# Kernel optimization log

Measured on AMD Instinct MI355X. Metric: run time of the kernel, lower is better.

## Reference

```python
import jax, jax.numpy as jnp
import numpy as np

B, C, L, N = 2, 8, 128, 48  # volume side L, kept size N per axis (fact=4 -> N >= L/4)


def setup_inputs() -> dict:
    key = jax.random.key(0)
    ks = jax.random.split(key, 7)
    x = jax.random.normal(ks[0], (B, C, L, L, L), dtype=jnp.float32)
    EN3 = jax.random.normal(ks[1], (L, N), dtype=jnp.float32)
    EN2 = jax.random.normal(ks[2], (L, N), dtype=jnp.float32)
    EN1 = jax.random.normal(ks[3], (L, N), dtype=jnp.float32)
    DE3 = jax.random.normal(ks[4], (N, L), dtype=jnp.float32)
    DE2 = jax.random.normal(ks[5], (N, L), dtype=jnp.float32)
    DE1 = jax.random.normal(ks[6], (N, L), dtype=jnp.float32)
    return {"x": x, "EN3": EN3, "EN2": EN2, "EN1": EN1,
            "DE3": DE3, "DE2": DE2, "DE1": DE1}


def reference(x, EN3, EN2, EN1, DE3, DE2, DE1):
    # ---- encode: contract D (axis -3) with EN3, H (axis -2) with EN2, W (axis -1) with EN1
    e = jnp.einsum('bcdhw,dp->bcphw', x, EN3)
    e = jnp.einsum('bcphw,hq->bcpqw', e, EN2)
    enc = jnp.einsum('bcpqw,wr->bcpqr', e, EN1)  # (B,C,N,N,N)
    # ---- decode: three application orders of DE1/DE2/DE3, averaged (as in source)
    # order W,H,D
    y = jnp.einsum('bcpqr,rw->bcpqw', enc, DE1)
    y = jnp.einsum('bcpqw,qh->bcphw', y, DE2)
    y1 = jnp.einsum('bcphw,pd->bcdhw', y, DE3)
    # order H,D,W
    y = jnp.einsum('bcpqr,qh->bcphr', enc, DE2)
    y = jnp.einsum('bcphr,pd->bcdhr', y, DE3)
    y2 = jnp.einsum('bcdhr,rw->bcdhw', y, DE1)
    # order D,W,H
    y = jnp.einsum('bcpqr,pd->bcdqr', enc, DE3)
    y = jnp.einsum('bcdqr,rw->bcdqw', y, DE1)
    y3 = jnp.einsum('bcdqw,qh->bcdhw', y, DE2)
    return (y1 + y2 + y3) / 3.0
```

## Files before the change

### kernel.cpp

```cpp
#include <hip/hip_runtime.h>


#define LDIM 128
#define NDIM 48
#define HW   (LDIM * LDIM)
#define L3V  (LDIM * HW)
#define QR   2304

typedef __bf16 bf16x8 __attribute__((ext_vector_type(8)));
typedef float  f32x4  __attribute__((ext_vector_type(4)));
typedef unsigned short u16;

#define S128 136
#define S64  72

#define W_EN3T 0
#define W_EN2T 6144
#define W_EN1T 12288
#define W_DE3T 18432
#define W_DE2T 26624
#define W_DE1T 34816
#define W_M    43008
#define W_TOT  59392

__device__ __forceinline__ u16 f2bf(float f) {
    unsigned int u = __builtin_bit_cast(unsigned int, f);
    return (u16)((u + 0x7fffu + ((u >> 16) & 1u)) >> 16);
}
__device__ __forceinline__ bf16x8 frag(const u16* p) {
    return *reinterpret_cast<const bf16x8*>(p);
}
__device__ __forceinline__ f32x4 mfma16(bf16x8 a, bf16x8 b, f32x4 c) {
    return __builtin_amdgcn_mfma_f32_16x16x32_bf16(a, b, c, 0, 0, 0);
}

__global__ __launch_bounds__(256) void kPrep(const float* __restrict__ EN3,
                                             const float* __restrict__ EN2,
                                             const float* __restrict__ EN1,
                                             const float* __restrict__ DE3,
                                             const float* __restrict__ DE2,
                                             const float* __restrict__ DE1,
                                             u16* __restrict__ W) {
    int i = blockIdx.x * 256 + threadIdx.x;
    if (i < 6144)       { int p = i >> 7, d = i & 127;                 W[i] = f2bf(EN3[d * 48 + p]); }
    else if (i < 12288) { int j = i - 6144;  int q = j >> 7, h = j & 127; W[i] = f2bf(EN2[h * 48 + q]); }
    else if (i < 18432) { int j = i - 12288; int r = j >> 7, w = j & 127; W[i] = f2bf(EN1[w * 48 + r]); }
    else if (i < 26624) { int j = i - 18432; int d = j >> 6, p = j & 63;  W[i] = f2bf(p < 48 ? DE3[p * 128 + d] : 0.f); }
    else if (i < 34816) { int j = i - 26624; int h = j >> 6, q = j & 63;  W[i] = f2bf(q < 48 ? DE2[q * 128 + h] : 0.f); }
    else if (i < 43008) { int j = i - 34816; int w = j >> 6, r = j & 63;  W[i] = f2bf(r < 48 ? DE1[r * 128 + w] : 0.f); }
    else if (i < 59392) {
        int j = i - 43008; int dp = j >> 7, d = j & 127;
        float s = 0.f;
        for (int p = 0; p < 48; ++p) s += EN3[d * 48 + p] * DE3[p * 128 + dp];
        W[i] = f2bf(s);
    }
}

__global__ __launch_bounds__(256) void kEnc(const float* __restrict__ x,
                                            const u16* __restrict__ W,
                                            u16* __restrict__ t) {
    __shared__ u16 lS[128 * S128];
    __shared__ u16 lT[48 * S128];
    const int bc = blockIdx.y, d = blockIdx.x;
    const int tid = threadIdx.x, lane = tid & 63, wv = tid >> 6, quad = lane >> 4;
    const int row = lane & 15, kof = quad * 8;

    {
        const float* xp = x + (size_t)bc * L3V + (size_t)d * HW;
        for (int i = 0; i < 16; ++i) {
            int f = i * 1024 + tid * 4;
            float4 v = *reinterpret_cast<const float4*>(xp + f);
            int h = f >> 7, w = f & 127;
            uint2 pk;
            pk.x = (unsigned)f2bf(v.x) | ((unsigned)f2bf(v.y) << 16);
            pk.y = (unsigned)f2bf(v.z) | ((unsigned)f2bf(v.w) << 16);
            *reinterpret_cast<uint2*>(lS + h * S128 + w) = pk;
        }
    }
    __syncthreads();
    {
        const int h0 = wv * 32;
        f32x4 acc[2][3] = {};
        for (int kk = 0; kk < 4; ++kk) {
            bf16x8 b[3];
            for (int n = 0; n < 3; ++n)
                b[n] = frag(W + W_EN1T + (n * 16 + row) * 128 + kk * 32 + kof);
            for (int m = 0; m < 2; ++m) {
                bf16x8 a = frag(lS + (h0 + m * 16 + row) * S128 + kk * 32 + kof);
                for (int n = 0; n < 3; ++n) acc[m][n] = mfma16(a, b[n], acc[m][n]);
            }
        }
        for (int m = 0; m < 2; ++m)
            for (int n = 0; n < 3; ++n) {
                int r = n * 16 + row, h = h0 + m * 16 + quad * 4;
                uint2 pk;
                pk.x = (unsigned)f2bf(acc[m][n][0]) | ((unsigned)f2bf(acc[m][n][1]) << 16);
                pk.y = (unsigned)f2bf(acc[m][n][2]) | ((unsigned)f2bf(acc[m][n][3]) << 16);
                *reinterpret_cast<uint2*>(lT + r * S128 + h) = pk;
            }
    }
    __syncthreads();
    if (wv < 3) {
        const int q0 = wv * 16;
        f32x4 acc[3] = {};
        for (int kk = 0; kk < 4; ++kk) {
            bf16x8 a = frag(W + W_EN2T + (q0 + row) * 128 + kk * 32 + kof);
            for (int n = 0; n < 3; ++n) {
                bf16x8 b = frag(lT + (n * 16 + row) * S128 + kk * 32 + kof);
                acc[n] = mfma16(a, b, acc[n]);
            }
        }
        u16* tp = t + (size_t)(bc * 128 + d) * QR;
        for (int n = 0; n < 3; ++n)
            for (int j = 0; j < 4; ++j)
                tp[(q0 + quad * 4 + j) * 48 + n * 16 + row] = f2bf(acc[n][j]);
    }
}

__global__ __launch_bounds__(256) void kM(const u16* __restrict__ t,
                                          const u16* __restrict__ W,
                                          u16* __restrict__ u) {
    __shared__ u16 lB[64 * S128];
    const int bc = blockIdx.y, qr0 = blockIdx.x * 64;
    const int tid = threadIdx.x, lane = tid & 63, wv = tid >> 6, quad = lane >> 4;
    const int row = lane & 15, kof = quad * 8;

    {
        const u16* tp = t + (size_t)bc * (128 * QR) + qr0 + (tid & 7) * 8;
        const int d0 = tid >> 3;
        for (int g = 0; g < 4; ++g) {
            int dd = d0 + g * 32;
            u16 v[8];
            *reinterpret_cast<float4*>(v) = *reinterpret_cast<const float4*>(tp + (size_t)dd * QR);
            for (int j = 0; j < 8; ++j) lB[((tid & 7) * 8 + j) * S128 + dd] = v[j];
        }
    }
    __syncthreads();
    const int m0 = wv * 32;
    f32x4 acc[2][4] = {};
    for (int kk = 0; kk < 4; ++kk) {
        bf16x8 a[2], b[4];
        for (int n = 0; n < 4; ++n)
            b[n] = frag(lB + (n * 16 + row) * S128 + kk * 32 + kof);
        for (int m = 0; m < 2; ++m)
            a[m] = frag(W + W_M + (m0 + m * 16 + row) * 128 + kk * 32 + kof);
        for (int m = 0; m < 2; ++m)
            for (int n = 0; n < 4; ++n) acc[m][n] = mfma16(a[m], b[n], acc[m][n]);
    }
    u16* up = u + (size_t)bc * (128 * QR) + qr0;
    for (int m = 0; m < 2; ++m)
        for (int n = 0; n < 4; ++n)
            for (int j = 0; j < 4; ++j) {
                int dp = m0 + m * 16 + quad * 4 + j;
                up[(size_t)dp * QR + n * 16 + row] = f2bf(acc[m][n][j]);
            }
}

__global__ __launch_bounds__(256) void kDec(const u16* __restrict__ u,
                                            const u16* __restrict__ W,
                                            float* __restrict__ out) {
    __shared__ u16 lU[48 * S64];
    __shared__ u16 lV[128 * S64];
    const int bc = blockIdx.y, dp = blockIdx.x;
    const int tid = threadIdx.x, lane = tid & 63, wv = tid >> 6, quad = lane >> 4;
    const int row = lane & 15, kof = quad * 8;

    for (int i = tid; i < 48 * 16; i += 256)  lU[(i >> 4) * S64 + 48 + (i & 15)] = 0;
    for (int i = tid; i < 128 * 16; i += 256) lV[(i >> 4) * S64 + 48 + (i & 15)] = 0;
    {
        const u16* sp = u + (size_t)(bc * 128 + dp) * QR;
        for (int i = tid; i < 288; i += 256) {
            u16 v[8];
            *reinterpret_cast<float4*>(v) = *reinterpret_cast<const float4*>(sp + i * 8);
            int q = i / 6, rb = (i % 6) * 8;
            for (int j = 0; j < 8; ++j) lU[(rb + j) * S64 + q] = v[j];
        }
    }
    __syncthreads();
    {
        const int h0 = wv * 32;
        f32x4 acc[2][3] = {};
        for (int kk = 0; kk < 2; ++kk) {
            bf16x8 b[3];
            for (int n = 0; n < 3; ++n)
                b[n] = frag(lU + (n * 16 + row) * S64 + kk * 32 + kof);
            for (int m = 0; m < 2; ++m) {
                bf16x8 a = frag(W + W_DE2T + (h0 + m * 16 + row) * 64 + kk * 32 + kof);
                for (int n = 0; n < 3; ++n) acc[m][n] = mfma16(a, b[n], acc[m][n]);
            }
        }
        for (int m = 0; m < 2; ++m)
            for (int n = 0; n < 3; ++n)
                for (int j = 0; j < 4; ++j)
                    lV[(h0 + m * 16 + quad * 4 + j) * S64 + n * 16 + row] = f2bf(acc[m][n][j]);
    }
    __syncthreads();
    {
        const int h0 = wv * 32;
        f32x4 acc[2][8] = {};
        for (int kk = 0; kk < 2; ++kk) {
            bf16x8 a[2], b[8];
            for (int n = 0; n < 8; ++n)
                b[n] = frag(W + W_DE1T + (n * 16 + row) * 64 + kk * 32 + kof);
            for (int m = 0; m < 2; ++m)
                a[m] = frag(lV + (h0 + m * 16 + row) * S64 + kk * 32 + kof);
            for (int m = 0; m < 2; ++m)
                for (int n = 0; n < 8; ++n) acc[m][n] = mfma16(a[m], b[n], acc[m][n]);
        }
        float* ob = out + (size_t)bc * L3V + (size_t)dp * HW;
        for (int m = 0; m < 2; ++m)
            for (int n = 0; n < 8; ++n)
                for (int j = 0; j < 4; ++j)
                    ob[(h0 + m * 16 + quad * 4 + j) * 128 + n * 16 + row] = acc[m][n][j];
    }
}

extern "C" void kernel_launch(void* const* d_in, const int* in_sizes, int n_in,
                              void* d_out, int out_size, void* d_ws, size_t ws_size,
                              hipStream_t stream) {
    const float* x   = (const float*)d_in[0];
    const float* EN3 = (const float*)d_in[1];
    const float* EN2 = (const float*)d_in[2];
    const float* EN1 = (const float*)d_in[3];
    const float* DE3 = (const float*)d_in[4];
    const float* DE2 = (const float*)d_in[5];
    const float* DE1 = (const float*)d_in[6];
    float* out = (float*)d_out;

    u16* t = (u16*)d_ws;
    u16* u = (u16*)((char*)d_ws + 9437184);
    u16* W = (u16*)((char*)d_ws + 18874368);

    kPrep<<<dim3(232),     256, 0, stream>>>(EN3, EN2, EN1, DE3, DE2, DE1, W);
    kEnc <<<dim3(128, 16), 256, 0, stream>>>(x, W, t);
    kM   <<<dim3(36, 16),  256, 0, stream>>>(t, W, u);
    kDec <<<dim3(128, 16), 256, 0, stream>>>(u, W, out);
}
```

Baseline: 279.6 us.

## Fold weight prep into each kernel and feed encoder MFMA straight from global

```diff
diff --git a/kernel.cpp b/kernel.cpp
--- a/kernel.cpp
+++ b/kernel.cpp
@@ -14,15 +14,6 @@
 #define S128 136
 #define S64  72
 
-#define W_EN3T 0
-#define W_EN2T 6144
-#define W_EN1T 12288
-#define W_DE3T 18432
-#define W_DE2T 26624
-#define W_DE1T 34816
-#define W_M    43008
-#define W_TOT  59392
-
 __device__ __forceinline__ u16 f2bf(float f) {
     unsigned int u = __builtin_bit_cast(unsigned int, f);
     return (u16)((u + 0x7fffu + ((u >> 16) & 1u)) >> 16);
@@ -34,59 +25,47 @@
     return __builtin_amdgcn_mfma_f32_16x16x32_bf16(a, b, c, 0, 0, 0);
 }
 
-__global__ __launch_bounds__(256) void kPrep(const float* __restrict__ EN3,
-                                             const float* __restrict__ EN2,
-                                             const float* __restrict__ EN1,
-                                             const float* __restrict__ DE3,
-                                             const float* __restrict__ DE2,
-                                             const float* __restrict__ DE1,
-                                             u16* __restrict__ W) {
-    int i = blockIdx.x * 256 + threadIdx.x;
-    if (i < 6144)       { int p = i >> 7, d = i & 127;                 W[i] = f2bf(EN3[d * 48 + p]); }
-    else if (i < 12288) { int j = i - 6144;  int q = j >> 7, h = j & 127; W[i] = f2bf(EN2[h * 48 + q]); }
-    else if (i < 18432) { int j = i - 12288; int r = j >> 7, w = j & 127; W[i] = f2bf(EN1[w * 48 + r]); }
-    else if (i < 26624) { int j = i - 18432; int d = j >> 6, p = j & 63;  W[i] = f2bf(p < 48 ? DE3[p * 128 + d] : 0.f); }
-    else if (i < 34816) { int j = i - 26624; int h = j >> 6, q = j & 63;  W[i] = f2bf(q < 48 ? DE2[q * 128 + h] : 0.f); }
-    else if (i < 43008) { int j = i - 34816; int w = j >> 6, r = j & 63;  W[i] = f2bf(r < 48 ? DE1[r * 128 + w] : 0.f); }
-    else if (i < 59392) {
-        int j = i - 43008; int dp = j >> 7, d = j & 127;
-        float s = 0.f;
-        for (int p = 0; p < 48; ++p) s += EN3[d * 48 + p] * DE3[p * 128 + dp];
-        W[i] = f2bf(s);
-    }
-}
-
 __global__ __launch_bounds__(256) void kEnc(const float* __restrict__ x,
-                                            const u16* __restrict__ W,
+                                            const float* __restrict__ EN1,
+                                            const float* __restrict__ EN2,
                                             u16* __restrict__ t) {
-    __shared__ u16 lS[128 * S128];
-    __shared__ u16 lT[48 * S128];
+    __shared__ u16 lW1[48 * S128];
+    __shared__ u16 lW2[48 * S128];
+    __shared__ u16 lT [48 * S128];
     const int bc = blockIdx.y, d = blockIdx.x;
     const int tid = threadIdx.x, lane = tid & 63, wv = tid >> 6, quad = lane >> 4;
     const int row = lane & 15, kof = quad * 8;
 
+    for (int i = tid; i < 1536; i += 256) {
+        int w = i / 12, g = i - w * 12, r0 = g * 4;
+        float4 v = *reinterpret_cast<const float4*>(EN1 + w * 48 + r0);
+        lW1[(r0 + 0) * S128 + w] = f2bf(v.x);
+        lW1[(r0 + 1) * S128 + w] = f2bf(v.y);
+        lW1[(r0 + 2) * S128 + w] = f2bf(v.z);
+        lW1[(r0 + 3) * S128 + w] = f2bf(v.w);
+        float4 u = *reinterpret_cast<const float4*>(EN2 + w * 48 + r0);
+        lW2[(r0 + 0) * S128 + w] = f2bf(u.x);
+        lW2[(r0 + 1) * S128 + w] = f2bf(u.y);
+        lW2[(r0 + 2) * S128 + w] = f2bf(u.z);
+        lW2[(r0 + 3) * S128 + w] = f2bf(u.w);
+    }
+    __syncthreads();
     {
         const float* xp = x + (size_t)bc * L3V + (size_t)d * HW;
-        for (int i = 0; i < 16; ++i) {
-            int f = i * 1024 + tid * 4;
-            float4 v = *reinterpret_cast<const float4*>(xp + f);
-            int h = f >> 7, w = f & 127;
-            uint2 pk;
-            pk.x = (unsigned)f2bf(v.x) | ((unsigned)f2bf(v.y) << 16);
-            pk.y = (unsigned)f2bf(v.z) | ((unsigned)f2bf(v.w) << 16);
-            *reinterpret_cast<uint2*>(lS + h * S128 + w) = pk;
-        }
-    }
-    __syncthreads();
-    {
         const int h0 = wv * 32;
         f32x4 acc[2][3] = {};
         for (int kk = 0; kk < 4; ++kk) {
             bf16x8 b[3];
             for (int n = 0; n < 3; ++n)
-                b[n] = frag(W + W_EN1T + (n * 16 + row) * 128 + kk * 32 + kof);
+                b[n] = frag(lW1 + (n * 16 + row) * S128 + kk * 32 + kof);
             for (int m = 0; m < 2; ++m) {
-                bf16x8 a = frag(lS + (h0 + m * 16 + row) * S128 + kk * 32 + kof);
+                const float* ap = xp + (h0 + m * 16 + row) * 128 + kk * 32 + kof;
+                float4 v0 = *reinterpret_cast<const float4*>(ap);
+                float4 v1 = *reinterpret_cast<const float4*>(ap + 4);
+                u16 av[8];
+                av[0] = f2bf(v0.x); av[1] = f2bf(v0.y); av[2] = f2bf(v0.z); av[3] = f2bf(v0.w);
+                av[4] = f2bf(v1.x); av[5] = f2bf(v1.y); av[6] = f2bf(v1.z); av[7] = f2bf(v1.w);
+                bf16x8 a = *reinterpret_cast<bf16x8*>(av);
                 for (int n = 0; n < 3; ++n) acc[m][n] = mfma16(a, b[n], acc[m][n]);
             }
         }
@@ -104,7 +83,7 @@
         const int q0 = wv * 16;
         f32x4 acc[3] = {};
         for (int kk = 0; kk < 4; ++kk) {
-            bf16x8 a = frag(W + W_EN2T + (q0 + row) * 128 + kk * 32 + kof);
+            bf16x8 a = frag(lW2 + (q0 + row) * S128 + kk * 32 + kof);
             for (int n = 0; n < 3; ++n) {
                 bf16x8 b = frag(lT + (n * 16 + row) * S128 + kk * 32 + kof);
                 acc[n] = mfma16(a, b, acc[n]);
@@ -117,14 +96,30 @@
     }
 }
 
-__global__ __launch_bounds__(256) void kM(const u16* __restrict__ t,
-                                          const u16* __restrict__ W,
-                                          u16* __restrict__ u) {
+__global__ __launch_bounds__(256) void kMD(const u16* __restrict__ t,
+                                           const float* __restrict__ EN3,
+                                           const float* __restrict__ DE3,
+                                           u16* __restrict__ u) {
+    __shared__ u16 lM[128 * S128];
     __shared__ u16 lB[64 * S128];
     const int bc = blockIdx.y, qr0 = blockIdx.x * 64;
     const int tid = threadIdx.x, lane = tid & 63, wv = tid >> 6, quad = lane >> 4;
     const int row = lane & 15, kof = quad * 8;
 
+    {
+        const int dp = tid & 127, d0 = (tid >> 7) * 64;
+        float de3[48];
+        for (int p = 0; p < 48; ++p) de3[p] = DE3[p * 128 + dp];
+        for (int dd = d0; dd < d0 + 64; ++dd) {
+            float s = 0.f;
+            for (int pv = 0; pv < 12; ++pv) {
+                float4 e = *reinterpret_cast<const float4*>(EN3 + dd * 48 + pv * 4);
+                s += e.x * de3[pv * 4 + 0] + e.y * de3[pv * 4 + 1]
+                   + e.z * de3[pv * 4 + 2] + e.w * de3[pv * 4 + 3];
+            }
+            lM[dp * S128 + dd] = f2bf(s);
+        }
+    }
     {
         const u16* tp = t + (size_t)bc * (128 * QR) + qr0 + (tid & 7) * 8;
         const int d0 = tid >> 3;
@@ -143,7 +138,7 @@
         for (int n = 0; n < 4; ++n)
             b[n] = frag(lB + (n * 16 + row) * S128 + kk * 32 + kof);
         for (int m = 0; m < 2; ++m)
-            a[m] = frag(W + W_M + (m0 + m * 16 + row) * 128 + kk * 32 + kof);
+            a[m] = frag(lM + (m0 + m * 16 + row) * S128 + kk * 32 + kof);
         for (int m = 0; m < 2; ++m)
             for (int n = 0; n < 4; ++n) acc[m][n] = mfma16(a[m], b[n], acc[m][n]);
     }
@@ -157,16 +152,35 @@
 }
 
 __global__ __launch_bounds__(256) void kDec(const u16* __restrict__ u,
-                                            const u16* __restrict__ W,
+                                            const float* __restrict__ DE2,
+                                            const float* __restrict__ DE1,
                                             float* __restrict__ out) {
-    __shared__ u16 lU[48 * S64];
-    __shared__ u16 lV[128 * S64];
+    __shared__ u16 lU  [48 * S64];
+    __shared__ u16 lV  [128 * S64];
+    __shared__ u16 lWD2[128 * S64];
+    __shared__ u16 lWD1[128 * S64];
     const int bc = blockIdx.y, dp = blockIdx.x;
     const int tid = threadIdx.x, lane = tid & 63, wv = tid >> 6, quad = lane >> 4;
     const int row = lane & 15, kof = quad * 8;
 
     for (int i = tid; i < 48 * 16; i += 256)  lU[(i >> 4) * S64 + 48 + (i & 15)] = 0;
-    for (int i = tid; i < 128 * 16; i += 256) lV[(i >> 4) * S64 + 48 + (i & 15)] = 0;
+    for (int i = tid; i < 128 * 16; i += 256) {
+        int rr = (i >> 4) * S64 + 48 + (i & 15);
+        lV[rr] = 0; lWD2[rr] = 0; lWD1[rr] = 0;
+    }
+    for (int i = tid; i < 1536; i += 256) {
+        int q = i >> 5, h0 = (i & 31) * 4;
+        float4 v = *reinterpret_cast<const float4*>(DE2 + q * 128 + h0);
+        lWD2[(h0 + 0) * S64 + q] = f2bf(v.x);
+        lWD2[(h0 + 1) * S64 + q] = f2bf(v.y);
+        lWD2[(h0 + 2) * S64 + q] = f2bf(v.z);
+        lWD2[(h0 + 3) * S64 + q] = f2bf(v.w);
+        float4 w = *reinterpret_cast<const float4*>(DE1 + q * 128 + h0);
+        lWD1[(h0 + 0) * S64 + q] = f2bf(w.x);
+        lWD1[(h0 + 1) * S64 + q] = f2bf(w.y);
+        lWD1[(h0 + 2) * S64 + q] = f2bf(w.z);
+        lWD1[(h0 + 3) * S64 + q] = f2bf(w.w);
+    }
     {
         const u16* sp = u + (size_t)(bc * 128 + dp) * QR;
         for (int i = tid; i < 288; i += 256) {
@@ -185,7 +199,7 @@
             for (int n = 0; n < 3; ++n)
                 b[n] = frag(lU + (n * 16 + row) * S64 + kk * 32 + kof);
             for (int m = 0; m < 2; ++m) {
-                bf16x8 a = frag(W + W_DE2T + (h0 + m * 16 + row) * 64 + kk * 32 + kof);
+                bf16x8 a = frag(lWD2 + (h0 + m * 16 + row) * S64 + kk * 32 + kof);
                 for (int n = 0; n < 3; ++n) acc[m][n] = mfma16(a, b[n], acc[m][n]);
             }
         }
@@ -201,7 +215,7 @@
         for (int kk = 0; kk < 2; ++kk) {
             bf16x8 a[2], b[8];
             for (int n = 0; n < 8; ++n)
-                b[n] = frag(W + W_DE1T + (n * 16 + row) * 64 + kk * 32 + kof);
+                b[n] = frag(lWD1 + (n * 16 + row) * S64 + kk * 32 + kof);
             for (int m = 0; m < 2; ++m)
                 a[m] = frag(lV + (h0 + m * 16 + row) * S64 + kk * 32 + kof);
             for (int m = 0; m < 2; ++m)
@@ -229,10 +243,8 @@
 
     u16* t = (u16*)d_ws;
     u16* u = (u16*)((char*)d_ws + 9437184);
-    u16* W = (u16*)((char*)d_ws + 18874368);
-
-    kPrep<<<dim3(232),     256, 0, stream>>>(EN3, EN2, EN1, DE3, DE2, DE1, W);
-    kEnc <<<dim3(128, 16), 256, 0, stream>>>(x, W, t);
-    kM   <<<dim3(36, 16),  256, 0, stream>>>(t, W, u);
-    kDec <<<dim3(128, 16), 256, 0, stream>>>(u, W, out);
-}
+
+    kEnc<<<dim3(128, 16), 256, 0, stream>>>(x, EN1, EN2, t);
+    kMD <<<dim3(36, 16),  256, 0, stream>>>(t, EN3, DE3, u);
+    kDec<<<dim3(128, 16), 256, 0, stream>>>(u, DE2, DE1, out);
+}
```

Result: slower. 348.3 us (+24.6%).
